# Kernel optimization log

Measured on AMD Instinct MI355X. Metric: run time of the kernel, lower is better.

The kernel has to match this reference:

```python
import jax, jax.numpy as jnp
import numpy as np

NEG_SLOPE = 0.01  # F.leaky_relu default
NUM_GRAPHS = 64


def sage_conv(x, src, dst, W_l, b_l, W_r):
    """PyG SAGEConv (mean aggr): lin_l(mean_j x_j) + lin_r(x_i)."""
    n = x.shape[0]
    msg = x[src]                                               # [E, C] gather
    agg = jax.ops.segment_sum(msg, dst, num_segments=n)        # [N, C] scatter-add
    deg = jax.ops.segment_sum(jnp.ones_like(dst, dtype=x.dtype), dst, num_segments=n)
    mean = agg / jnp.maximum(deg, 1.0)[:, None]
    return mean @ W_l + b_l + x @ W_r


def setup_inputs() -> dict:
    key = jax.random.key(0)
    ks = jax.random.split(key, 12)
    N, E, C, H, O = 50000, 600000, 128, 128, 2
    x = jax.random.normal(ks[0], (N, C), dtype=jnp.float32)
    edge_index = jax.random.randint(ks[1], (2, E), 0, N, dtype=jnp.int64)
    batch = jnp.sort(jax.random.randint(ks[2], (N,), 0, NUM_GRAPHS, dtype=jnp.int64))

    def lin(k, fin, fout):
        return jax.random.normal(k, (fin, fout), dtype=jnp.float32) / np.sqrt(fin)

    return {
        "x": x, "edge_index": edge_index, "batch": batch,
        "W1_l": lin(ks[3], C, H), "b1": jnp.zeros((H,), jnp.float32), "W1_r": lin(ks[4], C, H),
        "W2_l": lin(ks[5], H, H), "b2": jnp.zeros((H,), jnp.float32), "W2_r": lin(ks[6], H, H),
        "W3_l": lin(ks[7], H, H), "b3": jnp.zeros((H,), jnp.float32), "W3_r": lin(ks[8], H, H),
        "W_fc": lin(ks[9], H, O), "b_fc": jnp.zeros((O,), jnp.float32),
    }


def reference(x, edge_index, batch, W1_l, b1, W1_r, W2_l, b2, W2_r,
              W3_l, b3, W3_r, W_fc, b_fc):
    src, dst = edge_index[0], edge_index[1]
    h = jax.nn.leaky_relu(sage_conv(x, src, dst, W1_l, b1, W1_r), NEG_SLOPE)
    h = jax.nn.leaky_relu(sage_conv(h, src, dst, W2_l, b2, W2_r), NEG_SLOPE)
    h = jax.nn.leaky_relu(sage_conv(h, src, dst, W3_l, b3, W3_r), NEG_SLOPE)
    pooled = jax.ops.segment_max(h, batch, num_segments=NUM_GRAPHS)  # global_max_pool
    return pooled @ W_fc + b_fc
```

## Files before the change

### kernel.cpp

```cpp
#include <hip/hip_runtime.h>
#include <hip/hip_bf16.h>

#define NEG_SLOPE 0.01f
#define C 128
#define NGRAPH 64

typedef short short8 __attribute__((ext_vector_type(8)));
typedef float f32x4 __attribute__((ext_vector_type(4)));
typedef unsigned short ushort;

__device__ __forceinline__ unsigned fmap(float x){
  unsigned b = __float_as_uint(x);
  return (b & 0x80000000u) ? ~b : (b | 0x80000000u);
}
__device__ __forceinline__ float funmap(unsigned k){
  return (k & 0x80000000u) ? __uint_as_float(k & 0x7FFFFFFFu) : __uint_as_float(~k);
}

__device__ __forceinline__ ushort bf16_rne(float a){
  unsigned u = __float_as_uint(a);
  return (ushort)((u + 0x7FFFu + ((u >> 16) & 1u)) >> 16);
}
__device__ __forceinline__ float b2f(ushort h){
  return __uint_as_float(((unsigned)h) << 16);
}

__device__ __forceinline__ void lds_dma16(const void* g, void* l){
  __builtin_amdgcn_global_load_lds(
      (const __attribute__((address_space(1))) unsigned int*)(void*)g,
      (__attribute__((address_space(3))) unsigned int*)(void*)l, 16, 0, 0);
}

__global__ void prep_kernel(const float* __restrict__ x, ushort* __restrict__ xb, int nx4,
                            const int* __restrict__ dst, int* __restrict__ deg, int E,
                            const float* __restrict__ W1l, const float* __restrict__ W1r,
                            const float* __restrict__ W2l, const float* __restrict__ W2r,
                            const float* __restrict__ W3l, const float* __restrict__ W3r,
                            short* __restrict__ B1, short* __restrict__ B2,
                            short* __restrict__ B3,
                            int nblk_x, int nblk_deg){
  int bid = blockIdx.x;
  if(bid < nblk_x){
    int i = (bid * 256 + threadIdx.x) * 4;
    if(i < nx4){
      float4 v = *(const float4*)(x + i);
      ushort4 r = make_ushort4(bf16_rne(v.x), bf16_rne(v.y), bf16_rne(v.z), bf16_rne(v.w));
      *(ushort4*)(xb + i) = r;
    }
    return;
  }
  bid -= nblk_x;
  if(bid < nblk_deg){
    int e = bid * 256 + threadIdx.x;
    if(e < E) atomicAdd(&deg[dst[e]], 1);
    return;
  }
  bid -= nblk_deg;
  int set = bid >> 7;
  int idx = (bid & 127) * 256 + threadIdx.x;
  const float* Wl = (set == 0) ? W1l : (set == 1) ? W2l : W3l;
  const float* Wr = (set == 0) ? W1r : (set == 1) ? W2r : W3r;
  short* Bpk      = (set == 0) ? B1  : (set == 1) ? B2  : B3;
  int k = idx >> 7, n = idx & 127;
  float w = (k < C) ? Wl[k * C + n] : Wr[(k - C) * C + n];
  ushort hi = bf16_rne(w);
  float r = w - b2f(hi);
  ushort lo = bf16_rne(r);
  int kstep = k >> 5, kg = (k >> 3) & 3, j = k & 7;
  int pos = ((kstep * 4 + kg) * C + n) * 8 + j;
  Bpk[pos] = (short)hi;
  Bpk[pos + 32768] = (short)lo;
}

__global__ void scan_block(const int* __restrict__ deg, int* __restrict__ incl,
                           int* __restrict__ bsum, int N){
  __shared__ int sm[1024];
  int t = threadIdx.x;
  int i = blockIdx.x * 1024 + t;
  int v = (i < N) ? deg[i] : 0;
  sm[t] = v;
  __syncthreads();
  for(int off = 1; off < 1024; off <<= 1){
    int a = (t >= off) ? sm[t - off] : 0;
    __syncthreads();
    sm[t] += a;
    __syncthreads();
  }
  if(i < N) incl[i] = sm[t];
  if(t == 1023) bsum[blockIdx.x] = sm[t];
}

__global__ void scan_bsum(const int* __restrict__ bsum, int* __restrict__ boff, int nb){
  __shared__ int sm[64];
  int t = threadIdx.x;
  sm[t] = (t < nb) ? bsum[t] : 0;
  __syncthreads();
  for(int off = 1; off < 64; off <<= 1){
    int a = (t >= off) ? sm[t - off] : 0;
    __syncthreads();
    sm[t] += a;
    __syncthreads();
  }
  if(t < nb) boff[t] = sm[t] - bsum[t];
}

__global__ void finalize_rows(const int* __restrict__ incl, const int* __restrict__ deg,
                              const int* __restrict__ boff, int* __restrict__ rows,
                              float* __restrict__ inv_deg, int N, int E){
  int i = blockIdx.x * blockDim.x + threadIdx.x;
  if(i < N){
    rows[i] = incl[i] - deg[i] + boff[i >> 10];
    inv_deg[i] = 1.0f / fmaxf((float)deg[i], 1.0f);
  }
  if(i == 0) rows[N] = E;
}

__global__ void csr_fill_kernel(const int* __restrict__ src, const int* __restrict__ dst,
                                const int* __restrict__ row_start, int* __restrict__ cursor,
                                int* __restrict__ csr, int E){
  int e = blockIdx.x * blockDim.x + threadIdx.x;
  if(e >= E) return;
  int d = dst[e];
  int p = atomicAdd(&cursor[d], 1);
  csr[row_start[d] + p] = src[e];
}

__global__ __launch_bounds__(256, 2) void layer_fused(
    const ushort* __restrict__ xin, const int* __restrict__ csr,
    const int* __restrict__ rowp, const float* __restrict__ inv_deg,
    const short* __restrict__ Bpk, const float* __restrict__ bias,
    ushort* __restrict__ Hout, int M,
    const int* __restrict__ batch, unsigned* __restrict__ pooled)
{
  __shared__ ushort Ms[64 * 136];
  __shared__ __align__(16) ushort Xs[64 * 32];
  int tid = threadIdx.x;
  int bm = blockIdx.x * 64;
  int lane = tid & 63;
  int wn = tid >> 6;
  int lg = lane >> 4;
  int lm = lane & 15;

  {
    int grp = tid >> 4, g15 = tid & 15, gbase = tid & 48;
    for(int nn = grp; nn < 64; nn += 16){
      int node = bm + nn;
      float a[8] = {0.f, 0.f, 0.f, 0.f, 0.f, 0.f, 0.f, 0.f};
      if(node < M){
        int beg = rowp[node], end = rowp[node + 1];
        for(int base = beg; base < end; base += 16){
          int cnt = end - base; if(cnt > 16) cnt = 16;
          int s_l = (base + g15 < end) ? csr[base + g15] : 0;
          int j = 0;
          for(; j + 4 <= cnt; j += 4){
            int s0 = __shfl(s_l, gbase + j + 0, 64);
            int s1 = __shfl(s_l, gbase + j + 1, 64);
            int s2 = __shfl(s_l, gbase + j + 2, 64);
            int s3 = __shfl(s_l, gbase + j + 3, 64);
            short8 v0 = *(const short8*)(xin + (long long)s0 * C + g15 * 8);
            short8 v1 = *(const short8*)(xin + (long long)s1 * C + g15 * 8);
            short8 v2 = *(const short8*)(xin + (long long)s2 * C + g15 * 8);
            short8 v3 = *(const short8*)(xin + (long long)s3 * C + g15 * 8);
#pragma unroll
            for(int k = 0; k < 8; k++){
              a[k] += b2f((ushort)v0[k]); a[k] += b2f((ushort)v1[k]);
              a[k] += b2f((ushort)v2[k]); a[k] += b2f((ushort)v3[k]);
            }
          }
          for(; j < cnt; j++){
            int s = __shfl(s_l, gbase + j, 64);
            short8 v = *(const short8*)(xin + (long long)s * C + g15 * 8);
#pragma unroll
            for(int k = 0; k < 8; k++) a[k] += b2f((ushort)v[k]);
          }
        }
        float sc = inv_deg[node];
#pragma unroll
        for(int k = 0; k < 8; k++) a[k] *= sc;
      }
      short8 o;
#pragma unroll
      for(int k = 0; k < 8; k++) o[k] = (short)bf16_rne(a[k]);
      *(short8*)(Ms + nn * 136 + g15 * 8) = o;
    }
  }

  int srow = tid >> 2;
  int sslice = (tid & 3) ^ ((tid >> 3) & 3);
  int grow = bm + srow; if(grow >= M) grow = M - 1;
  const long long goff = (long long)grow * C + sslice * 8;
  ushort* ldsbase = Xs + wn * 512;

  f32x4 acc[4][2];
#pragma unroll
  for(int i = 0; i < 4; i++)
#pragma unroll
    for(int j = 0; j < 2; j++)
      acc[i][j] = (f32x4){0.f, 0.f, 0.f, 0.f};

  short8 bh[2][2], bl[2][2];
  auto loadB = [&](int ks, int buf){
#pragma unroll
    for(int j = 0; j < 2; j++){
      const short* bp = Bpk + (((ks * 4 + lg) * C) + wn * 32 + j * 16 + lm) * 8;
      bh[buf][j] = *(const short8*)bp;
      bl[buf][j] = *(const short8*)(bp + 32768);
    }
  };
  loadB(0, 0);
  __syncthreads();

#pragma unroll
  for(int ks = 0; ks < 8; ks++){
    if(ks >= 4){
      if(ks > 4) __syncthreads();
      lds_dma16(xin + goff + (ks - 4) * 32, ldsbase);
    }
    if(ks < 7) loadB(ks + 1, (ks + 1) & 1);
    if(ks >= 4) __syncthreads();

    short8 af[4];
    if(ks < 4){
#pragma unroll
      for(int i = 0; i < 4; i++)
        af[i] = *(const short8*)(Ms + (i * 16 + lm) * 136 + ks * 32 + lg * 8);
    }else{
#pragma unroll
      for(int i = 0; i < 4; i++){
        int r = i * 16 + lm;
        int slot = lg ^ ((r >> 1) & 3);
        af[i] = *(const short8*)(Xs + r * 32 + slot * 8);
      }
    }
    int b = ks & 1;
#pragma unroll
    for(int i = 0; i < 4; i++)
#pragma unroll
      for(int j = 0; j < 2; j++){
        acc[i][j] = __builtin_amdgcn_mfma_f32_16x16x32_bf16(af[i], bh[b][j], acc[i][j], 0, 0, 0);
        acc[i][j] = __builtin_amdgcn_mfma_f32_16x16x32_bf16(af[i], bl[b][j], acc[i][j], 0, 0, 0);
      }
  }

  if(pooled == nullptr){
#pragma unroll
    for(int j = 0; j < 2; j++){
      int col = wn * 32 + j * 16 + lm;
      float bv = bias[col];
#pragma unroll
      for(int i = 0; i < 4; i++){
#pragma unroll
        for(int reg = 0; reg < 4; reg++){
          int row = bm + i * 16 + lg * 4 + reg;
          if(row < M){
            float v = acc[i][j][reg] + bv;
            v = v > 0.f ? v : NEG_SLOPE * v;
            Hout[(long long)row * C + col] = bf16_rne(v);
          }
        }
      }
    }
  }else{
#pragma unroll
    for(int i = 0; i < 4; i++){
      int row0 = bm + i * 16 + lg * 4;
      if(row0 >= M) continue;
      bool whole = (row0 + 3 < M);
      int g0 = batch[row0];
      bool same = whole && (batch[row0 + 3] == g0);
#pragma unroll
      for(int j = 0; j < 2; j++){
        int col = wn * 32 + j * 16 + lm;
        float bv = bias[col];
        float v0 = acc[i][j][0] + bv; v0 = v0 > 0.f ? v0 : NEG_SLOPE * v0;
        float v1 = acc[i][j][1] + bv; v1 = v1 > 0.f ? v1 : NEG_SLOPE * v1;
        float v2 = acc[i][j][2] + bv; v2 = v2 > 0.f ? v2 : NEG_SLOPE * v2;
        float v3 = acc[i][j][3] + bv; v3 = v3 > 0.f ? v3 : NEG_SLOPE * v3;
        if(same){
          float m01 = fmaxf(v0, v1), m23 = fmaxf(v2, v3);
          atomicMax(&pooled[g0 * C + col], fmap(fmaxf(m01, m23)));
        }else{
          float vv[4] = {v0, v1, v2, v3};
#pragma unroll
          for(int reg = 0; reg < 4; reg++){
            int row = row0 + reg;
            if(row < M) atomicMax(&pooled[batch[row] * C + col], fmap(vv[reg]));
          }
        }
      }
    }
  }
}

__global__ void fc_kernel(const unsigned* __restrict__ pooled_u, const float* __restrict__ Wfc,
                          const float* __restrict__ bfc, float* __restrict__ out){
  int t = threadIdx.x;
  int g = t >> 1, o = t & 1;
  float s = bfc[o];
  for(int k = 0; k < C; k++)
    s += funmap(pooled_u[g * C + k]) * Wfc[k * 2 + o];
  out[g * 2 + o] = s;
}

extern "C" void kernel_launch(void* const* d_in, const int* in_sizes, int n_in,
                              void* d_out, int out_size, void* d_ws, size_t ws_size,
                              hipStream_t stream) {
  const float* x    = (const float*)d_in[0];
  const int*   ei   = (const int*)d_in[1];
  const int*   batch= (const int*)d_in[2];
  const float* W1l  = (const float*)d_in[3];
  const float* b1   = (const float*)d_in[4];
  const float* W1r  = (const float*)d_in[5];
  const float* W2l  = (const float*)d_in[6];
  const float* b2   = (const float*)d_in[7];
  const float* W2r  = (const float*)d_in[8];
  const float* W3l  = (const float*)d_in[9];
  const float* b3   = (const float*)d_in[10];
  const float* W3r  = (const float*)d_in[11];
  const float* Wfc  = (const float*)d_in[12];
  const float* bfc  = (const float*)d_in[13];
  float* out = (float*)d_out;

  const int N = in_sizes[0] / C;
  const int E = in_sizes[1] / 2;
  const int* srcv = ei;
  const int* dstv = ei + E;

  char* ws = (char*)d_ws;
  size_t off = 0;
  auto alloc = [&](size_t bytes) -> void* {
    void* p = ws + off;
    off += (bytes + 255) & ~(size_t)255;
    return p;
  };
  int*      deg    = (int*)alloc((size_t)N * 4);
  int*      cursor = (int*)alloc((size_t)N * 4);
  unsigned* pooled = (unsigned*)alloc((size_t)NGRAPH * C * 4);
  size_t    zbytes = off;
  float*    inv_d  = (float*)alloc((size_t)N * 4);
  int*      incl   = (int*)alloc((size_t)N * 4);
  int*      bsum   = (int*)alloc((size_t)64 * 4);
  int*      boff   = (int*)alloc((size_t)64 * 4);
  int*      rows   = (int*)alloc((size_t)(N + 1) * 4);
  int*      csr    = (int*)alloc((size_t)E * 4);
  ushort*   xb     = (ushort*)alloc((size_t)N * C * 2);
  ushort*   h1b    = (ushort*)alloc((size_t)N * C * 2);
  short*    B1     = (short*)alloc((size_t)2 * 2 * C * C * 2);
  short*    B2     = (short*)alloc((size_t)2 * 2 * C * C * 2);
  short*    B3     = (short*)alloc((size_t)2 * 2 * C * C * 2);

  hipMemsetAsync(deg, 0, zbytes, stream);

  const int nbx  = (N * C / 4 + 255) / 256;
  const int nbd  = (E + 255) / 256;
  const int nbp  = 3 * 128;
  prep_kernel<<<nbx + nbd + nbp, 256, 0, stream>>>(
      x, xb, N * C, dstv, deg, E,
      W1l, W1r, W2l, W2r, W3l, W3r, B1, B2, B3, nbx, nbd);

  const int nb = (N + 1023) / 1024;
  scan_block<<<nb, 1024, 0, stream>>>(deg, incl, bsum, N);
  scan_bsum<<<1, 64, 0, stream>>>(bsum, boff, nb);
  finalize_rows<<<(N + 255) / 256, 256, 0, stream>>>(incl, deg, boff, rows, inv_d, N, E);
  csr_fill_kernel<<<(E + 255) / 256, 256, 0, stream>>>(srcv, dstv, rows, cursor, csr, E);

  int lblocks = (N + 63) / 64;

  layer_fused<<<lblocks, 256, 0, stream>>>(xb, csr, rows, inv_d, B1, b1,
                                           h1b, N, nullptr, nullptr);
  layer_fused<<<lblocks, 256, 0, stream>>>(h1b, csr, rows, inv_d, B2, b2,
                                           xb, N, nullptr, nullptr);
  layer_fused<<<lblocks, 256, 0, stream>>>(xb, csr, rows, inv_d, B3, b3,
                                           nullptr, N, batch, pooled);

  fc_kernel<<<1, 128, 0, stream>>>(pooled, Wfc, bfc, out);
}
```

Baseline: 287.2 us.

## Fuse CSR build preprocessing into one cooperative kernel with grid syncs

Replaces the memset, prep, block scan, bsum scan, finalize and CSR fill launches with a single cooperative kernel of 256 blocks that uses grid-wide syncs between phases. This removes five launches and the gaps between them. In exchange, only 256 blocks do all the elementwise and atomic work through grid-stride loops. That may underutilize the GPU for the large bf16 conversion and the edge atomics, and each grid sync adds its own cost.

```diff
diff --git a/kernel.cpp b/kernel.cpp
--- a/kernel.cpp
+++ b/kernel.cpp
@@ -1,5 +1,8 @@
 #include <hip/hip_runtime.h>
 #include <hip/hip_bf16.h>
+#include <hip/hip_cooperative_groups.h>
+
+namespace cg = cooperative_groups;
 
 #define NEG_SLOPE 0.01f
 #define C 128
@@ -31,98 +34,93 @@
       (__attribute__((address_space(3))) unsigned int*)(void*)l, 16, 0, 0);
 }
 
-__global__ void prep_kernel(const float* __restrict__ x, ushort* __restrict__ xb, int nx4,
-                            const int* __restrict__ dst, int* __restrict__ deg, int E,
-                            const float* __restrict__ W1l, const float* __restrict__ W1r,
-                            const float* __restrict__ W2l, const float* __restrict__ W2r,
-                            const float* __restrict__ W3l, const float* __restrict__ W3r,
-                            short* __restrict__ B1, short* __restrict__ B2,
-                            short* __restrict__ B3,
-                            int nblk_x, int nblk_deg){
-  int bid = blockIdx.x;
-  if(bid < nblk_x){
-    int i = (bid * 256 + threadIdx.x) * 4;
-    if(i < nx4){
-      float4 v = *(const float4*)(x + i);
-      ushort4 r = make_ushort4(bf16_rne(v.x), bf16_rne(v.y), bf16_rne(v.z), bf16_rne(v.w));
-      *(ushort4*)(xb + i) = r;
-    }
-    return;
-  }
-  bid -= nblk_x;
-  if(bid < nblk_deg){
-    int e = bid * 256 + threadIdx.x;
-    if(e < E) atomicAdd(&deg[dst[e]], 1);
-    return;
-  }
-  bid -= nblk_deg;
-  int set = bid >> 7;
-  int idx = (bid & 127) * 256 + threadIdx.x;
-  const float* Wl = (set == 0) ? W1l : (set == 1) ? W2l : W3l;
-  const float* Wr = (set == 0) ? W1r : (set == 1) ? W2r : W3r;
-  short* Bpk      = (set == 0) ? B1  : (set == 1) ? B2  : B3;
-  int k = idx >> 7, n = idx & 127;
-  float w = (k < C) ? Wl[k * C + n] : Wr[(k - C) * C + n];
-  ushort hi = bf16_rne(w);
-  float r = w - b2f(hi);
-  ushort lo = bf16_rne(r);
-  int kstep = k >> 5, kg = (k >> 3) & 3, j = k & 7;
-  int pos = ((kstep * 4 + kg) * C + n) * 8 + j;
-  Bpk[pos] = (short)hi;
-  Bpk[pos + 32768] = (short)lo;
-}
-
-__global__ void scan_block(const int* __restrict__ deg, int* __restrict__ incl,
-                           int* __restrict__ bsum, int N){
-  __shared__ int sm[1024];
-  int t = threadIdx.x;
-  int i = blockIdx.x * 1024 + t;
-  int v = (i < N) ? deg[i] : 0;
-  sm[t] = v;
-  __syncthreads();
-  for(int off = 1; off < 1024; off <<= 1){
-    int a = (t >= off) ? sm[t - off] : 0;
+__global__ void build_kernel(
+    const float* __restrict__ x, ushort* __restrict__ xb, int nquads,
+    const int* __restrict__ src, const int* __restrict__ dst, int E,
+    int* __restrict__ deg, int* __restrict__ cursor, unsigned* __restrict__ pooled,
+    int* __restrict__ incl, int* __restrict__ bsum, int* __restrict__ boff,
+    int* __restrict__ rows, float* __restrict__ inv_deg, int* __restrict__ csr, int N,
+    const float* __restrict__ W1l, const float* __restrict__ W1r,
+    const float* __restrict__ W2l, const float* __restrict__ W2r,
+    const float* __restrict__ W3l, const float* __restrict__ W3r,
+    short* __restrict__ B1, short* __restrict__ B2, short* __restrict__ B3)
+{
+  cg::grid_group grid = cg::this_grid();
+  __shared__ int sm[256];
+  const int t = threadIdx.x;
+  const int gtid = blockIdx.x * 256 + t;
+  const int gsz = gridDim.x * 256;
+  const int nt = (N + 255) >> 8;
+
+  for(int i = gtid; i < N; i += gsz){ deg[i] = 0; cursor[i] = 0; }
+  for(int i = gtid; i < NGRAPH * C; i += gsz) pooled[i] = 0u;
+  grid.sync();
+
+  for(int i = gtid; i < nquads; i += gsz){
+    float4 v = *(const float4*)(x + (long long)i * 4);
+    ushort4 r = make_ushort4(bf16_rne(v.x), bf16_rne(v.y), bf16_rne(v.z), bf16_rne(v.w));
+    *(ushort4*)(xb + (long long)i * 4) = r;
+  }
+  for(int idx = gtid; idx < 3 * 2 * C * C; idx += gsz){
+    int set = idx >> 15;
+    int w_i = idx & 32767;
+    const float* Wl = (set == 0) ? W1l : (set == 1) ? W2l : W3l;
+    const float* Wr = (set == 0) ? W1r : (set == 1) ? W2r : W3r;
+    short* Bpk      = (set == 0) ? B1  : (set == 1) ? B2  : B3;
+    int k = w_i >> 7, n = w_i & 127;
+    float w = (k < C) ? Wl[k * C + n] : Wr[(k - C) * C + n];
+    ushort hi = bf16_rne(w);
+    float r = w - b2f(hi);
+    ushort lo = bf16_rne(r);
+    int kstep = k >> 5, kg = (k >> 3) & 3, j = k & 7;
+    int pos = ((kstep * 4 + kg) * C + n) * 8 + j;
+    Bpk[pos] = (short)hi;
+    Bpk[pos + 32768] = (short)lo;
+  }
+  for(int e = gtid; e < E; e += gsz) atomicAdd(&deg[dst[e]], 1);
+  grid.sync();
+
+  for(int tile = blockIdx.x; tile < nt; tile += gridDim.x){
+    int i = tile * 256 + t;
+    int v = (i < N) ? deg[i] : 0;
+    sm[t] = v;
     __syncthreads();
-    sm[t] += a;
+    for(int off = 1; off < 256; off <<= 1){
+      int a = (t >= off) ? sm[t - off] : 0;
+      __syncthreads();
+      sm[t] += a;
+      __syncthreads();
+    }
+    if(i < N) incl[i] = sm[t];
+    if(t == 255) bsum[tile] = sm[255];
     __syncthreads();
   }
-  if(i < N) incl[i] = sm[t];
-  if(t == 1023) bsum[blockIdx.x] = sm[t];
-}
-
-__global__ void scan_bsum(const int* __restrict__ bsum, int* __restrict__ boff, int nb){
-  __shared__ int sm[64];
-  int t = threadIdx.x;
-  sm[t] = (t < nb) ? bsum[t] : 0;
-  __syncthreads();
-  for(int off = 1; off < 64; off <<= 1){
-    int a = (t >= off) ? sm[t - off] : 0;
+  grid.sync();
+
+  if(blockIdx.x == 0){
+    int v = (t < nt) ? bsum[t] : 0;
+    sm[t] = v;
     __syncthreads();
-    sm[t] += a;
-    __syncthreads();
-  }
-  if(t < nb) boff[t] = sm[t] - bsum[t];
-}
-
-__global__ void finalize_rows(const int* __restrict__ incl, const int* __restrict__ deg,
-                              const int* __restrict__ boff, int* __restrict__ rows,
-                              float* __restrict__ inv_deg, int N, int E){
-  int i = blockIdx.x * blockDim.x + threadIdx.x;
-  if(i < N){
-    rows[i] = incl[i] - deg[i] + boff[i >> 10];
+    for(int off = 1; off < 256; off <<= 1){
+      int a = (t >= off) ? sm[t - off] : 0;
+      __syncthreads();
+      sm[t] += a;
+      __syncthreads();
+    }
+    if(t < nt) boff[t] = sm[t] - v;
+  }
+  grid.sync();
+
+  for(int i = gtid; i < N; i += gsz){
+    rows[i] = incl[i] - deg[i] + boff[i >> 8];
     inv_deg[i] = 1.0f / fmaxf((float)deg[i], 1.0f);
   }
-  if(i == 0) rows[N] = E;
-}
-
-__global__ void csr_fill_kernel(const int* __restrict__ src, const int* __restrict__ dst,
-                                const int* __restrict__ row_start, int* __restrict__ cursor,
-                                int* __restrict__ csr, int E){
-  int e = blockIdx.x * blockDim.x + threadIdx.x;
-  if(e >= E) return;
-  int d = dst[e];
-  int p = atomicAdd(&cursor[d], 1);
-  csr[row_start[d] + p] = src[e];
+  if(gtid == 0) rows[N] = E;
+  for(int e = gtid; e < E; e += gsz){
+    int d = dst[e];
+    int p = atomicAdd(&cursor[d], 1);
+    csr[incl[d] - deg[d] + boff[d >> 8] + p] = src[e];
+  }
 }
 
 __global__ __launch_bounds__(256, 2) void layer_fused(
@@ -336,11 +334,10 @@
   int*      deg    = (int*)alloc((size_t)N * 4);
   int*      cursor = (int*)alloc((size_t)N * 4);
   unsigned* pooled = (unsigned*)alloc((size_t)NGRAPH * C * 4);
-  size_t    zbytes = off;
   float*    inv_d  = (float*)alloc((size_t)N * 4);
   int*      incl   = (int*)alloc((size_t)N * 4);
-  int*      bsum   = (int*)alloc((size_t)64 * 4);
-  int*      boff   = (int*)alloc((size_t)64 * 4);
+  int*      bsum   = (int*)alloc((size_t)256 * 4);
+  int*      boff   = (int*)alloc((size_t)256 * 4);
   int*      rows   = (int*)alloc((size_t)(N + 1) * 4);
   int*      csr    = (int*)alloc((size_t)E * 4);
   ushort*   xb     = (ushort*)alloc((size_t)N * C * 2);
@@ -349,20 +346,20 @@
   short*    B2     = (short*)alloc((size_t)2 * 2 * C * C * 2);
   short*    B3     = (short*)alloc((size_t)2 * 2 * C * C * 2);
 
-  hipMemsetAsync(deg, 0, zbytes, stream);
-
-  const int nbx  = (N * C / 4 + 255) / 256;
-  const int nbd  = (E + 255) / 256;
-  const int nbp  = 3 * 128;
-  prep_kernel<<<nbx + nbd + nbp, 256, 0, stream>>>(
-      x, xb, N * C, dstv, deg, E,
-      W1l, W1r, W2l, W2r, W3l, W3r, B1, B2, B3, nbx, nbd);
-
-  const int nb = (N + 1023) / 1024;
-  scan_block<<<nb, 1024, 0, stream>>>(deg, incl, bsum, N);
-  scan_bsum<<<1, 64, 0, stream>>>(bsum, boff, nb);
-  finalize_rows<<<(N + 255) / 256, 256, 0, stream>>>(incl, deg, boff, rows, inv_d, N, E);
-  csr_fill_kernel<<<(E + 255) / 256, 256, 0, stream>>>(srcv, dstv, rows, cursor, csr, E);
+  int nquads = N * C / 4;
+  int Ev = E, Nv = N;
+  void* args[] = {
+    (void*)&x, (void*)&xb, (void*)&nquads,
+    (void*)&srcv, (void*)&dstv, (void*)&Ev,
+    (void*)&deg, (void*)&cursor, (void*)&pooled,
+    (void*)&incl, (void*)&bsum, (void*)&boff,
+    (void*)&rows, (void*)&inv_d, (void*)&csr, (void*)&Nv,
+    (void*)&W1l, (void*)&W1r, (void*)&W2l, (void*)&W2r,
+    (void*)&W3l, (void*)&W3r,
+    (void*)&B1, (void*)&B2, (void*)&B3
+  };
+  hipLaunchCooperativeKernel((void*)build_kernel, dim3(256), dim3(256),
+                             args, 0, stream);
 
   int lblocks = (N + 63) / 64;
 
```

Result: slower. 411.8 us (+43.4%).
